# Optimization experiments

Hardware: AMD Instinct MI355X
Metric: run time of the kernel (lower is better)

Reference implementation:

```python
import jax, jax.numpy as jnp
import numpy as np

N, E = 100000, 1600000
DIM, H, D = 64, 4, 8          # dim, num_heads, qk_dim
DH = D * H                    # 32
QK_SCALE = (DIM // H) ** -0.5


def setup_inputs() -> dict:
    key = jax.random.key(0)
    k1, k2, k3, k4 = jax.random.split(key, 4)
    x = jax.random.normal(k1, (N, DIM), dtype=jnp.float32)
    edge_index = jax.random.randint(k2, (2, E), 0, N, dtype=jnp.int64)
    W_qkv = jax.random.normal(k3, (DIM, 2 * DH + DIM), dtype=jnp.float32) * (DIM ** -0.5)
    b_qkv = jax.random.normal(k4, (2 * DH + DIM,), dtype=jnp.float32) * 0.02
    return {"x": x, "edge_index": edge_index, "W_qkv": W_qkv, "b_qkv": b_qkv}


def reference(x, edge_index, W_qkv, b_qkv):
    n = x.shape[0]
    e = edge_index.shape[1]
    qkv = x @ W_qkv + b_qkv                       # (N, 2*DH+DIM)
    q = qkv[:, :DH].reshape(n, H, D)
    k = qkv[:, DH:2 * DH].reshape(n, H, D)
    v = qkv[:, 2 * DH:].reshape(n, H, DIM // H)
    s, t = edge_index[0], edge_index[1]
    q_e = q[s] * QK_SCALE                         # (E, H, D)
    k_e = k[t]
    v_e = v[t]                                    # (E, H, DIM/H)
    # scale q by 1/sqrt(num source neighbors) (bincount of s)
    deg = jax.ops.segment_sum(jnp.ones((e,), x.dtype), s, num_segments=n)
    q_e = q_e * (deg[s] ** -0.5)[:, None, None]
    compat = jnp.einsum('ehd,ehd->eh', q_e, k_e)  # (E, H)
    # segment softmax over edges grouped by source node s
    m = jax.ops.segment_max(compat, s, num_segments=n)
    ex = jnp.exp(compat - m[s])
    denom = jax.ops.segment_sum(ex, s, num_segments=n)
    attn = ex / (denom[s] + 1e-16)                # (E, H)
    msg = (v_e * attn[..., None]).reshape(e, DIM)  # (E, DIM)
    out = jax.ops.segment_sum(msg, s, num_segments=n)  # (N, DIM)
    return out
```

## Files before the change

### kernel.cpp

```cpp
#include <hip/hip_runtime.h>


#define NDIM 64
#define NBMAX 1024
#define CTILE 8192
#define STGMAX 4352

static __device__ __forceinline__ unsigned short f2bf(float f) {
    unsigned int u = __float_as_uint(f);
    unsigned int r = (u + 0x7fffu + ((u >> 16) & 1u)) >> 16;
    return (unsigned short)r;
}

__global__ void bucket_count_kernel(const int* __restrict__ s_arr,
                                    unsigned int* __restrict__ bcnt, int E) {
    __shared__ unsigned int h[NBMAX];
    for (int i = threadIdx.x; i < NBMAX; i += blockDim.x) h[i] = 0;
    __syncthreads();
    int i0 = blockIdx.x * blockDim.x + threadIdx.x;
    int st = gridDim.x * blockDim.x;
    for (int e = i0; e < E; e += st)
        atomicAdd(&h[(unsigned)s_arr[e] >> 7], 1u);
    __syncthreads();
    for (int i = threadIdx.x; i < NBMAX; i += blockDim.x)
        if (h[i]) atomicAdd(&bcnt[i], h[i]);
}

__global__ void scan_buckets_kernel(const unsigned int* __restrict__ bcnt,
                                    unsigned int* __restrict__ bbase,
                                    unsigned int* __restrict__ gcur) {
    __shared__ unsigned int sh[1024];
    int tid = threadIdx.x;
    unsigned int v = bcnt[tid];
    unsigned int acc = v;
    sh[tid] = acc;
    __syncthreads();
    for (int off = 1; off < 1024; off <<= 1) {
        unsigned int add = (tid >= off) ? sh[tid - off] : 0;
        __syncthreads();
        acc += add;
        sh[tid] = acc;
        __syncthreads();
    }
    bbase[tid] = acc - v;
    gcur[tid]  = acc - v;
}

__global__ void bin_kernel(const int* __restrict__ s_arr,
                           const int* __restrict__ t_arr,
                           unsigned int* __restrict__ gcur,
                           unsigned int* __restrict__ binned, int E) {
    __shared__ unsigned int hist[NBMAX];
    __shared__ unsigned int off[NBMAX];
    __shared__ unsigned int gbase[NBMAX];
    __shared__ unsigned int stg[CTILE];
    __shared__ unsigned int psum[512];
    int tid = threadIdx.x;
    int e0 = blockIdx.x * CTILE;
    int cnt = min(CTILE, E - e0);

    for (int i = tid; i < NBMAX; i += 512) hist[i] = 0;
    __syncthreads();
    for (int i = tid; i < cnt; i += 512)
        atomicAdd(&hist[(unsigned)s_arr[e0 + i] >> 7], 1u);
    __syncthreads();

    unsigned int a0 = hist[2 * tid];
    unsigned int a1 = hist[2 * tid + 1];
    unsigned int ps = a0 + a1;
    unsigned int acc = ps;
    psum[tid] = acc;
    __syncthreads();
    for (int o = 1; o < 512; o <<= 1) {
        unsigned int add = (tid >= o) ? psum[tid - o] : 0;
        __syncthreads();
        acc += add;
        psum[tid] = acc;
        __syncthreads();
    }
    unsigned int exc = acc - ps;
    off[2 * tid]     = exc;
    off[2 * tid + 1] = exc + a0;
    __syncthreads();

    for (int i = tid; i < cnt; i += 512) {
        int s = s_arr[e0 + i];
        int t = t_arr[e0 + i];
        unsigned int bkt = (unsigned)s >> 7;
        unsigned int p = atomicAdd(&off[bkt], 1u);
        stg[p] = ((unsigned)(s & 127) << 17) | (unsigned)t;
    }
    __syncthreads();

    for (int i = tid; i < NBMAX; i += 512) {
        unsigned int h = hist[i];
        gbase[i] = h ? atomicAdd(&gcur[i], h) : 0u;
    }
    __syncthreads();

    int wid = tid >> 6, lane = tid & 63;
    for (int b = wid; b < NBMAX; b += 8) {
        unsigned int h = hist[b];
        if (h == 0) continue;
        unsigned int src = off[b] - h;
        unsigned int dst = gbase[b];
        for (unsigned int i = lane; i < h; i += 64)
            binned[dst + i] = stg[src + i];
    }
}

__global__ void qkv_gemm_kernel(const float* __restrict__ x,
                                const float* __restrict__ W,
                                const float* __restrict__ b,
                                float* __restrict__ qs,
                                unsigned short* __restrict__ kv, int N) {
    int col = threadIdx.x & 127;
    int rw  = threadIdx.x >> 7;
    float w[64];
    #pragma unroll
    for (int k = 0; k < 64; ++k) w[k] = W[k * 128 + col];
    float bias = b[col];
    __shared__ float4 xs[2][16];

    for (int r0 = blockIdx.x * 2; r0 < N; r0 += gridDim.x * 2) {
        __syncthreads();
        if (threadIdx.x < 32) {
            int rr = threadIdx.x >> 4;
            int cc = threadIdx.x & 15;
            int n = r0 + rr;
            xs[rr][cc] = (n < N)
                ? reinterpret_cast<const float4*>(x)[(size_t)n * 16 + cc]
                : make_float4(0.f, 0.f, 0.f, 0.f);
        }
        __syncthreads();
        int n = r0 + rw;
        if (n < N) {
            float acc = bias;
            #pragma unroll
            for (int k4 = 0; k4 < 16; ++k4) {
                float4 xv = xs[rw][k4];
                acc = fmaf(xv.x, w[4 * k4 + 0], acc);
                acc = fmaf(xv.y, w[4 * k4 + 1], acc);
                acc = fmaf(xv.z, w[4 * k4 + 2], acc);
                acc = fmaf(xv.w, w[4 * k4 + 3], acc);
            }
            if (col < 32) {
                qs[(size_t)n * 32 + col] = acc;
            } else if (col < 64) {
                kv[(size_t)n * 96 + (col - 32)] = f2bf(acc);
            } else {
                kv[(size_t)n * 96 + 32 + (col - 64)] = f2bf(acc);
            }
        }
    }
}

__global__ void __launch_bounds__(1024, 2)
sort_aggregate_kernel(const unsigned int* __restrict__ bbase,
                      const unsigned int* __restrict__ bcnt,
                      const unsigned int* __restrict__ binned,
                      const float* __restrict__ qs,
                      const unsigned int* __restrict__ kv32,
                      float* __restrict__ out, int N) {
    __shared__ unsigned int hist[128];
    __shared__ unsigned int rstart[128];
    __shared__ unsigned int cur[128];
    __shared__ unsigned int sh[128];
    __shared__ unsigned int stg[STGMAX];

    int b = blockIdx.x;
    int tid = threadIdx.x;
    unsigned int base = bbase[b];
    unsigned int cnt = min(bcnt[b], (unsigned int)STGMAX);

    if (tid < 128) hist[tid] = 0;
    __syncthreads();
    for (unsigned int i = tid; i < cnt; i += 1024)
        atomicAdd(&hist[binned[base + i] >> 17], 1u);
    __syncthreads();

    unsigned int v = (tid < 128) ? hist[tid] : 0;
    unsigned int acc = v;
    if (tid < 128) sh[tid] = acc;
    __syncthreads();
    for (int o = 1; o < 128; o <<= 1) {
        unsigned int add = (tid >= o && tid < 128) ? sh[tid - o] : 0;
        __syncthreads();
        if (tid < 128) { acc += add; sh[tid] = acc; }
        __syncthreads();
    }
    if (tid < 128) {
        unsigned int exc = acc - v;
        rstart[tid] = exc;
        cur[tid] = exc;
    }
    __syncthreads();

    for (unsigned int i = tid; i < cnt; i += 1024) {
        unsigned int e = binned[base + i];
        unsigned int p = atomicAdd(&cur[e >> 17], 1u);
        stg[p] = e & 0x1FFFFu;
    }
    __syncthreads();

    int wid = tid >> 6, lane = tid & 63;
    int csrc = (lane < 16) ? (lane & ~3)
             : (lane < 48) ? (((lane - 16) >> 3) << 2)
                           : 0;

    for (int nl = wid * 8; nl < wid * 8 + 8; ++nl) {
        int n = b * 128 + nl;
        if (n >= N) break;
        int dg = (int)hist[nl];
        if (dg == 0) {
            if (lane >= 16 && lane < 48)
                *reinterpret_cast<float2*>(&out[(size_t)n * 64 + 2 * (lane - 16)]) =
                    make_float2(0.f, 0.f);
            continue;
        }
        int start = (int)rstart[nl];
        int end = start + dg;
        float sc = 0.25f * rsqrtf((float)dg);
        float q0 = 0.f, q1 = 0.f;
        if (lane < 16) {
            q0 = qs[(size_t)n * 32 + 2 * lane] * sc;
            q1 = qs[(size_t)n * 32 + 2 * lane + 1] * sc;
        }

        float accx = 0.f, accy = 0.f, den = 0.f;
        int j = start;
        for (; j + 3 < end; j += 4) {
            unsigned int t0 = stg[j], t1 = stg[j + 1];
            unsigned int t2 = stg[j + 2], t3 = stg[j + 3];
            unsigned int r0 = 0, r1 = 0, r2 = 0, r3 = 0;
            if (lane < 48) {
                r0 = kv32[(size_t)t0 * 48 + lane];
                r1 = kv32[(size_t)t1 * 48 + lane];
                r2 = kv32[(size_t)t2 * 48 + lane];
                r3 = kv32[(size_t)t3 * 48 + lane];
            }
            float lo0 = __uint_as_float(r0 << 16), hi0 = __uint_as_float(r0 & 0xffff0000u);
            float lo1 = __uint_as_float(r1 << 16), hi1 = __uint_as_float(r1 & 0xffff0000u);
            float lo2 = __uint_as_float(r2 << 16), hi2 = __uint_as_float(r2 & 0xffff0000u);
            float lo3 = __uint_as_float(r3 << 16), hi3 = __uint_as_float(r3 & 0xffff0000u);
            float p0 = fmaf(q0, lo0, q1 * hi0);
            float p1 = fmaf(q0, lo1, q1 * hi1);
            float p2 = fmaf(q0, lo2, q1 * hi2);
            float p3 = fmaf(q0, lo3, q1 * hi3);
            p0 += __shfl_xor(p0, 1); p0 += __shfl_xor(p0, 2);
            p1 += __shfl_xor(p1, 1); p1 += __shfl_xor(p1, 2);
            p2 += __shfl_xor(p2, 1); p2 += __shfl_xor(p2, 2);
            p3 += __shfl_xor(p3, 1); p3 += __shfl_xor(p3, 2);
            float c0 = __shfl(p0, csrc), c1 = __shfl(p1, csrc);
            float c2 = __shfl(p2, csrc), c3 = __shfl(p3, csrc);
            float w0 = __expf(c0), w1 = __expf(c1);
            float w2 = __expf(c2), w3 = __expf(c3);
            accx = fmaf(w0, lo0, accx); accy = fmaf(w0, hi0, accy);
            accx = fmaf(w1, lo1, accx); accy = fmaf(w1, hi1, accy);
            accx = fmaf(w2, lo2, accx); accy = fmaf(w2, hi2, accy);
            accx = fmaf(w3, lo3, accx); accy = fmaf(w3, hi3, accy);
            den += (w0 + w1) + (w2 + w3);
        }
        for (; j < end; ++j) {
            unsigned int t0 = stg[j];
            unsigned int r0 = 0;
            if (lane < 48) r0 = kv32[(size_t)t0 * 48 + lane];
            float lo0 = __uint_as_float(r0 << 16), hi0 = __uint_as_float(r0 & 0xffff0000u);
            float p0 = fmaf(q0, lo0, q1 * hi0);
            p0 += __shfl_xor(p0, 1); p0 += __shfl_xor(p0, 2);
            float c0 = __shfl(p0, csrc);
            float w0 = __expf(c0);
            accx = fmaf(w0, lo0, accx); accy = fmaf(w0, hi0, accy);
            den += w0;
        }
        if (lane >= 16 && lane < 48) {
            float inv = 1.0f / (den + 1e-16f);
            float2 o = make_float2(accx * inv, accy * inv);
            *reinterpret_cast<float2*>(&out[(size_t)n * 64 + 2 * (lane - 16)]) = o;
        }
    }
}

extern "C" void kernel_launch(void* const* d_in, const int* in_sizes, int n_in,
                              void* d_out, int out_size, void* d_ws, size_t ws_size,
                              hipStream_t stream) {
    const float* x = (const float*)d_in[0];
    const int*   eidx = (const int*)d_in[1];
    const float* W = (const float*)d_in[2];
    const float* b = (const float*)d_in[3];
    int N = in_sizes[0] / NDIM;
    int E = in_sizes[1] / 2;
    float* out = (float*)d_out;

    int NB = (N + 127) / 128;

    float* qs = (float*)d_ws;
    unsigned short* kv = (unsigned short*)(qs + (size_t)N * 32);
    unsigned int* bcnt  = (unsigned int*)(kv + (size_t)N * 96);
    unsigned int* bbase = bcnt + NBMAX;
    unsigned int* gcur  = bbase + NBMAX;
    unsigned int* binned = gcur + NBMAX;

    const int* s_arr = eidx;
    const int* t_arr = eidx + E;

    hipMemsetAsync(bcnt, 0, NBMAX * sizeof(unsigned int), stream);

    bucket_count_kernel<<<256, 256, 0, stream>>>(s_arr, bcnt, E);
    scan_buckets_kernel<<<1, 1024, 0, stream>>>(bcnt, bbase, gcur);
    bin_kernel<<<(E + CTILE - 1) / CTILE, 512, 0, stream>>>(s_arr, t_arr, gcur, binned, E);
    qkv_gemm_kernel<<<2048, 256, 0, stream>>>(x, W, b, qs, kv, N);
    sort_aggregate_kernel<<<NB, 1024, 0, stream>>>(
        bbase, bcnt, binned, qs, (const unsigned int*)kv, out, N);
}
```

Baseline: 196.1 us.

## Widen bin kernel to 1024 threads, batch GEMM rows, deepen gather unroll

The bin kernel moves to 1024 threads, so each thread owns one bucket in the scan and in the global-offset atomics. The QKV GEMM now processes 8 rows per block iteration, 4 per thread, so each weight register set is reused across more rows. The aggregation loop adds an 8-way unrolled gather with 32-bit index arithmetic to put more kv loads in flight, and the bucket count kernel launches twice as many blocks. These raise memory-level parallelism and cut per-row synchronisation, at the cost of more registers and a longer serial scan.

```diff
diff --git a/kernel.cpp b/kernel.cpp
--- a/kernel.cpp
+++ b/kernel.cpp
@@ -46,44 +46,41 @@
     gcur[tid]  = acc - v;
 }
 
-__global__ void bin_kernel(const int* __restrict__ s_arr,
-                           const int* __restrict__ t_arr,
-                           unsigned int* __restrict__ gcur,
-                           unsigned int* __restrict__ binned, int E) {
+__global__ void __launch_bounds__(1024, 2)
+bin_kernel(const int* __restrict__ s_arr,
+           const int* __restrict__ t_arr,
+           unsigned int* __restrict__ gcur,
+           unsigned int* __restrict__ binned, int E) {
     __shared__ unsigned int hist[NBMAX];
     __shared__ unsigned int off[NBMAX];
     __shared__ unsigned int gbase[NBMAX];
     __shared__ unsigned int stg[CTILE];
-    __shared__ unsigned int psum[512];
+    __shared__ unsigned int psum[NBMAX];
     int tid = threadIdx.x;
     int e0 = blockIdx.x * CTILE;
     int cnt = min(CTILE, E - e0);
 
-    for (int i = tid; i < NBMAX; i += 512) hist[i] = 0;
-    __syncthreads();
-    for (int i = tid; i < cnt; i += 512)
+    hist[tid] = 0;
+    __syncthreads();
+    for (int i = tid; i < cnt; i += 1024)
         atomicAdd(&hist[(unsigned)s_arr[e0 + i] >> 7], 1u);
     __syncthreads();
 
-    unsigned int a0 = hist[2 * tid];
-    unsigned int a1 = hist[2 * tid + 1];
-    unsigned int ps = a0 + a1;
-    unsigned int acc = ps;
+    unsigned int v = hist[tid];
+    unsigned int acc = v;
     psum[tid] = acc;
     __syncthreads();
-    for (int o = 1; o < 512; o <<= 1) {
+    for (int o = 1; o < 1024; o <<= 1) {
         unsigned int add = (tid >= o) ? psum[tid - o] : 0;
         __syncthreads();
         acc += add;
         psum[tid] = acc;
         __syncthreads();
     }
-    unsigned int exc = acc - ps;
-    off[2 * tid]     = exc;
-    off[2 * tid + 1] = exc + a0;
-    __syncthreads();
-
-    for (int i = tid; i < cnt; i += 512) {
+    off[tid] = acc - v;
+    __syncthreads();
+
+    for (int i = tid; i < cnt; i += 1024) {
         int s = s_arr[e0 + i];
         int t = t_arr[e0 + i];
         unsigned int bkt = (unsigned)s >> 7;
@@ -92,14 +89,14 @@
     }
     __syncthreads();
 
-    for (int i = tid; i < NBMAX; i += 512) {
-        unsigned int h = hist[i];
-        gbase[i] = h ? atomicAdd(&gcur[i], h) : 0u;
+    {
+        unsigned int h = hist[tid];
+        gbase[tid] = h ? atomicAdd(&gcur[tid], h) : 0u;
     }
     __syncthreads();
 
     int wid = tid >> 6, lane = tid & 63;
-    for (int b = wid; b < NBMAX; b += 8) {
+    for (int b = wid; b < NBMAX; b += 16) {
         unsigned int h = hist[b];
         if (h == 0) continue;
         unsigned int src = off[b] - h;
@@ -120,11 +117,11 @@
     #pragma unroll
     for (int k = 0; k < 64; ++k) w[k] = W[k * 128 + col];
     float bias = b[col];
-    __shared__ float4 xs[2][16];
-
-    for (int r0 = blockIdx.x * 2; r0 < N; r0 += gridDim.x * 2) {
-        __syncthreads();
-        if (threadIdx.x < 32) {
+    __shared__ float4 xs[8][16];
+
+    for (int r0 = blockIdx.x * 8; r0 < N; r0 += gridDim.x * 8) {
+        __syncthreads();
+        if (threadIdx.x < 128) {
             int rr = threadIdx.x >> 4;
             int cc = threadIdx.x & 15;
             int n = r0 + rr;
@@ -133,23 +130,27 @@
                 : make_float4(0.f, 0.f, 0.f, 0.f);
         }
         __syncthreads();
-        int n = r0 + rw;
-        if (n < N) {
-            float acc = bias;
-            #pragma unroll
-            for (int k4 = 0; k4 < 16; ++k4) {
-                float4 xv = xs[rw][k4];
-                acc = fmaf(xv.x, w[4 * k4 + 0], acc);
-                acc = fmaf(xv.y, w[4 * k4 + 1], acc);
-                acc = fmaf(xv.z, w[4 * k4 + 2], acc);
-                acc = fmaf(xv.w, w[4 * k4 + 3], acc);
-            }
-            if (col < 32) {
-                qs[(size_t)n * 32 + col] = acc;
-            } else if (col < 64) {
-                kv[(size_t)n * 96 + (col - 32)] = f2bf(acc);
-            } else {
-                kv[(size_t)n * 96 + 32 + (col - 64)] = f2bf(acc);
+        #pragma unroll
+        for (int rsub = 0; rsub < 4; ++rsub) {
+            int rr = rw * 4 + rsub;
+            int n = r0 + rr;
+            if (n < N) {
+                float acc = bias;
+                #pragma unroll
+                for (int k4 = 0; k4 < 16; ++k4) {
+                    float4 xv = xs[rr][k4];
+                    acc = fmaf(xv.x, w[4 * k4 + 0], acc);
+                    acc = fmaf(xv.y, w[4 * k4 + 1], acc);
+                    acc = fmaf(xv.z, w[4 * k4 + 2], acc);
+                    acc = fmaf(xv.w, w[4 * k4 + 3], acc);
+                }
+                if (col < 32) {
+                    qs[(size_t)n * 32 + col] = acc;
+                } else if (col < 64) {
+                    kv[(size_t)n * 96 + (col - 32)] = f2bf(acc);
+                } else {
+                    kv[(size_t)n * 96 + 32 + (col - 64)] = f2bf(acc);
+                }
             }
         }
     }
@@ -204,6 +205,7 @@
     __syncthreads();
 
     int wid = tid >> 6, lane = tid & 63;
+    unsigned int ulane = (unsigned int)lane;
     int csrc = (lane < 16) ? (lane & ~3)
              : (lane < 48) ? (((lane - 16) >> 3) << 2)
                            : 0;
@@ -229,49 +231,68 @@
 
         float accx = 0.f, accy = 0.f, den = 0.f;
         int j = start;
+        for (; j + 7 < end; j += 8) {
+            unsigned int t[8], r[8];
+            #pragma unroll
+            for (int i = 0; i < 8; ++i) t[i] = stg[j + i];
+            #pragma unroll
+            for (int i = 0; i < 8; ++i)
+                r[i] = (lane < 48) ? kv32[t[i] * 48u + ulane] : 0u;
+            float lo[8], hi[8], p[8];
+            #pragma unroll
+            for (int i = 0; i < 8; ++i) {
+                lo[i] = __uint_as_float(r[i] << 16);
+                hi[i] = __uint_as_float(r[i] & 0xffff0000u);
+                p[i] = fmaf(q0, lo[i], q1 * hi[i]);
+            }
+            #pragma unroll
+            for (int i = 0; i < 8; ++i) {
+                p[i] += __shfl_xor(p[i], 1);
+                p[i] += __shfl_xor(p[i], 2);
+            }
+            #pragma unroll
+            for (int i = 0; i < 8; ++i) {
+                float c = __shfl(p[i], csrc);
+                float w = __expf(c);
+                accx = fmaf(w, lo[i], accx);
+                accy = fmaf(w, hi[i], accy);
+                den += w;
+            }
+        }
         for (; j + 3 < end; j += 4) {
-            unsigned int t0 = stg[j], t1 = stg[j + 1];
-            unsigned int t2 = stg[j + 2], t3 = stg[j + 3];
-            unsigned int r0 = 0, r1 = 0, r2 = 0, r3 = 0;
-            if (lane < 48) {
-                r0 = kv32[(size_t)t0 * 48 + lane];
-                r1 = kv32[(size_t)t1 * 48 + lane];
-                r2 = kv32[(size_t)t2 * 48 + lane];
-                r3 = kv32[(size_t)t3 * 48 + lane];
-            }
-            float lo0 = __uint_as_float(r0 << 16), hi0 = __uint_as_float(r0 & 0xffff0000u);
-            float lo1 = __uint_as_float(r1 << 16), hi1 = __uint_as_float(r1 & 0xffff0000u);
-            float lo2 = __uint_as_float(r2 << 16), hi2 = __uint_as_float(r2 & 0xffff0000u);
-            float lo3 = __uint_as_float(r3 << 16), hi3 = __uint_as_float(r3 & 0xffff0000u);
-            float p0 = fmaf(q0, lo0, q1 * hi0);
-            float p1 = fmaf(q0, lo1, q1 * hi1);
-            float p2 = fmaf(q0, lo2, q1 * hi2);
-            float p3 = fmaf(q0, lo3, q1 * hi3);
-            p0 += __shfl_xor(p0, 1); p0 += __shfl_xor(p0, 2);
-            p1 += __shfl_xor(p1, 1); p1 += __shfl_xor(p1, 2);
-            p2 += __shfl_xor(p2, 1); p2 += __shfl_xor(p2, 2);
-            p3 += __shfl_xor(p3, 1); p3 += __shfl_xor(p3, 2);
-            float c0 = __shfl(p0, csrc), c1 = __shfl(p1, csrc);
-            float c2 = __shfl(p2, csrc), c3 = __shfl(p3, csrc);
-            float w0 = __expf(c0), w1 = __expf(c1);
-            float w2 = __expf(c2), w3 = __expf(c3);
-            accx = fmaf(w0, lo0, accx); accy = fmaf(w0, hi0, accy);
-            accx = fmaf(w1, lo1, accx); accy = fmaf(w1, hi1, accy);
-            accx = fmaf(w2, lo2, accx); accy = fmaf(w2, hi2, accy);
-            accx = fmaf(w3, lo3, accx); accy = fmaf(w3, hi3, accy);
-            den += (w0 + w1) + (w2 + w3);
+            unsigned int t[4], r[4];
+            #pragma unroll
+            for (int i = 0; i < 4; ++i) t[i] = stg[j + i];
+            #pragma unroll
+            for (int i = 0; i < 4; ++i)
+                r[i] = (lane < 48) ? kv32[t[i] * 48u + ulane] : 0u;
+            #pragma unroll
+            for (int i = 0; i < 4; ++i) {
+                float lo = __uint_as_float(r[i] << 16);
+                float hi = __uint_as_float(r[i] & 0xffff0000u);
+                float p = fmaf(q0, lo, q1 * hi);
+                p += __shfl_xor(p, 1);
+                p += __shfl_xor(p, 2);
+                float c = __shfl(p, csrc);
+                float w = __expf(c);
+                accx = fmaf(w, lo, accx);
+                accy = fmaf(w, hi, accy);
+                den += w;
+            }
         }
         for (; j < end; ++j) {
             unsigned int t0 = stg[j];
-            unsigned int r0 = 0;
-            if (lane < 48) r0 = kv32[(size_t)t0 * 48 + lane];
-            float lo0 = __uint_as_float(r0 << 16), hi0 = __uint_as_float(r0 & 0xffff0000u);
-            float p0 = fmaf(q0, lo0, q1 * hi0);
-            p0 += __shfl_xor(p0, 1); p0 += __shfl_xor(p0, 2);
-            float c0 = __shfl(p0, csrc);
-            float w0 = __expf(c0);
-            accx = fmaf(w0, lo0, accx); accy = fmaf(w0, hi0, accy);
-            den += w0;
+            unsigned int r0 = (lane < 48) ? kv32[t0 * 48u + ulane] : 0u;
+            float lo = __uint_as_float(r0 << 16);
+            float hi = __uint_as_float(r0 & 0xffff0000u);
+            float p = fmaf(q0, lo, q1 * hi);
+            p += __shfl_xor(p, 1);
+            p += __shfl_xor(p, 2);
+            float c = __shfl(p, csrc);
+            float w = __expf(c);
+            accx = fmaf(w, lo, accx);
+            accy = fmaf(w, hi, accy);
+            den += w;
         }
         if (lane >= 16 && lane < 48) {
             float inv = 1.0f / (den + 1e-16f);
@@ -306,9 +327,9 @@
 
     hipMemsetAsync(bcnt, 0, NBMAX * sizeof(unsigned int), stream);
 
-    bucket_count_kernel<<<256, 256, 0, stream>>>(s_arr, bcnt, E);
+    bucket_count_kernel<<<512, 256, 0, stream>>>(s_arr, bcnt, E);
     scan_buckets_kernel<<<1, 1024, 0, stream>>>(bcnt, bbase, gcur);
-    bin_kernel<<<(E + CTILE - 1) / CTILE, 512, 0, stream>>>(s_arr, t_arr, gcur, binned, E);
+    bin_kernel<<<(E + CTILE - 1) / CTILE, 1024, 0, stream>>>(s_arr, t_arr, gcur, binned, E);
     qkv_gemm_kernel<<<2048, 256, 0, stream>>>(x, W, b, qs, kv, N);
     sort_aggregate_kernel<<<NB, 1024, 0, stream>>>(
         bbase, bcnt, binned, qs, (const unsigned int*)kv, out, N);
```

Result: faster. 177.0 us (-9.7%).
